# Optimization experiments

Hardware: AMD Instinct MI355X
Metric: run time of the kernel (lower is better)

Reference implementation:

```python
import jax, jax.numpy as jnp
from jax import lax
import numpy as np

B, T, D, H, DH, FF, K = 16, 1024, 512, 8, 64, 2048, 3
EPS = 1e-5


def _layer_norm(x, g, b):
    mu = jnp.mean(x, axis=-1, keepdims=True)
    var = jnp.mean((x - mu) ** 2, axis=-1, keepdims=True)
    return (x - mu) / jnp.sqrt(var + EPS) * g + b


def setup_inputs() -> dict:
    key = jax.random.key(0)
    ks = jax.random.split(key, 14)
    f32 = jnp.float32
    dec_inp = jax.random.normal(ks[0], (B, T, D), f32)
    lengths = jax.random.randint(ks[1], (B,), T // 2, T + 1)
    mask = (jnp.arange(T)[None, :] < lengths[:, None])[:, :, None]  # [B,T,1] bool
    qkv_w = jax.random.normal(ks[2], (3 * H * DH, D), f32) * (D ** -0.5)
    qkv_b = jnp.zeros((3 * H * DH,), f32)
    o_w = jax.random.normal(ks[3], (D, H * DH), f32) * ((H * DH) ** -0.5)
    ln1_g = jnp.ones((D,), f32)
    ln1_b = jnp.zeros((D,), f32)
    conv1_w = jax.random.normal(ks[4], (FF, D, K), f32) * ((D * K) ** -0.5)
    conv1_b = jnp.zeros((FF,), f32)
    conv2_w = jax.random.normal(ks[5], (D, FF, K), f32) * ((FF * K) ** -0.5)
    conv2_b = jnp.zeros((D,), f32)
    ln2_g = jnp.ones((D,), f32)
    ln2_b = jnp.zeros((D,), f32)
    return dict(dec_inp=dec_inp, mask=mask, qkv_w=qkv_w, qkv_b=qkv_b, o_w=o_w,
                ln1_g=ln1_g, ln1_b=ln1_b, conv1_w=conv1_w, conv1_b=conv1_b,
                conv2_w=conv2_w, conv2_b=conv2_b, ln2_g=ln2_g, ln2_b=ln2_b)


def reference(dec_inp, mask, qkv_w, qkv_b, o_w, ln1_g, ln1_b,
              conv1_w, conv1_b, conv2_w, conv2_b, ln2_g, ln2_b):
    # ----- MultiHeadAttn (post-norm, dropout = identity in eval) -----
    attn_mask = ~mask[:, :, 0]                      # [B,T], True = pad
    qkv = dec_inp @ qkv_w.T + qkv_b                 # [B,T,3*H*DH]
    q, k, v = jnp.split(qkv, 3, axis=2)

    def to_heads(x):  # [B,T,H*DH] -> [B*H,T,DH] (batch-major, as in torch)
        return x.reshape(B, T, H, DH).transpose(0, 2, 1, 3).reshape(B * H, T, DH)

    q, k, v = to_heads(q), to_heads(k), to_heads(v)
    scores = jnp.einsum('bqd,bkd->bqk', q, k) * (DH ** -0.5)  # [B*H,T,T]
    # faithful to torch: mask tiled head-major (index i % B)
    am = jnp.tile(attn_mask[:, None, :], (H, T, 1))           # [B*H,T,T]
    scores = jnp.where(am, -jnp.inf, scores)
    prob = jax.nn.softmax(scores, axis=2)
    vec = jnp.einsum('bqk,bkd->bqd', prob, v)                 # [B*H,T,DH]
    # faithful to torch: view as [H,B,...] then permute
    vec = vec.reshape(H, B, T, DH).transpose(1, 2, 0, 3).reshape(B, T, H * DH)
    attn_out = vec @ o_w.T                                    # [B,T,D]
    out = _layer_norm(dec_inp + attn_out, ln1_g, ln1_b)
    out = out * mask

    # ----- PositionwiseConvFF (post-norm) -----
    x = out.transpose(0, 2, 1)                                # [B,D,T]
    h = lax.conv_general_dilated(x, conv1_w, (1,), [(K // 2, K // 2)],
                                 dimension_numbers=('NCH', 'OIH', 'NCH'))
    h = jax.nn.relu(h + conv1_b[None, :, None])
    h = lax.conv_general_dilated(h, conv2_w, (1,), [(K // 2, K // 2)],
                                 dimension_numbers=('NCH', 'OIH', 'NCH'))
    core = (h + conv2_b[None, :, None]).transpose(0, 2, 1)    # [B,T,D]
    out = _layer_norm(out + core, ln2_g, ln2_b)
    return out * mask
```

## Files before the change

### kernel.cpp

```cpp
#include <hip/hip_runtime.h>

using h16 = _Float16;
using h16x4 = __attribute__((ext_vector_type(4))) _Float16;
using h16x8 = __attribute__((ext_vector_type(8))) _Float16;
using f32x4 = __attribute__((ext_vector_type(4))) float;

static constexpr int cB = 16, cT = 1024, cD = 512, cH = 8, cDH = 64, cFF = 2048;
static constexpr int cM = cB * cT;
static constexpr int cTP = cT + 2;

__device__ __forceinline__ bool mask_val(const void* mb, int idx) {
  const unsigned char* u8 = (const unsigned char*)mb;
  if (u8[1] == 1) return u8[idx] != 0;
  const float* f = (const float*)mb;
  if (f[1] == 1.0f) return f[idx] != 0.0f;
  return ((const int*)mb)[idx] != 0;
}

__device__ __forceinline__ void gl_lds16(const h16* g, h16* l) {
  __builtin_amdgcn_global_load_lds(
      (const __attribute__((address_space(1))) unsigned int*)g,
      (__attribute__((address_space(3))) unsigned int*)l, 16, 0, 0);
}


__global__ __launch_bounds__(256) void k_cast4(const float* __restrict__ in,
                                               h16* __restrict__ out, int n4) {
  int i = blockIdx.x * 256 + threadIdx.x;
  if (i >= n4) return;
  const float4 f = ((const float4*)in)[i];
  h16x4 o = {(h16)f.x, (h16)f.y, (h16)f.z, (h16)f.w};
  ((h16x4*)out)[i] = o;
}

__global__ __launch_bounds__(256) void k_repack_w1(const float* __restrict__ w,
                                                   h16* __restrict__ out) {
  int i = blockIdx.x * 256 + threadIdx.x;
  if (i >= cFF * cD) return;
  int f = i >> 9, d = i & 511;
#pragma unroll
  for (int k = 0; k < 3; ++k)
    out[f * (3 * cD) + k * cD + d] = (h16)w[(long)i * 3 + k];
}

__global__ __launch_bounds__(256) void k_repack_w2(const float* __restrict__ w,
                                                   h16* __restrict__ out) {
  int i = blockIdx.x * 256 + threadIdx.x;
  if (i >= cD * cFF) return;
  int o = i >> 11, f = i & 2047;
#pragma unroll
  for (int k = 0; k < 3; ++k)
    out[o * (3 * cFF) + k * cFF + f] = (h16)w[(long)i * 3 + k];
}

__global__ __launch_bounds__(256) void k_zero_pads(h16* __restrict__ xp,
                                                   h16* __restrict__ hp) {
  int i = blockIdx.x * 256 + threadIdx.x;
  if (i < cB * 2 * cD) {
    int b = i / (2 * cD); int rr = (i / cD) & 1; int c = i % cD;
    xp[((long)b * cTP + rr * (cTP - 1)) * cD + c] = (h16)0.f;
  }
  if (i < cB * 2 * cFF) {
    int b = i / (2 * cFF); int rr = (i / cFF) & 1; int c = i % cFF;
    hp[((long)b * cTP + rr * (cTP - 1)) * cFF + c] = (h16)0.f;
  }
}

template <int SKIP, bool A_CONV, bool OUT_CONV, bool BIAS, bool RELU,
          bool OUT_H16, bool VSCAT, int SPLITK, bool SWIZ>
__global__ __launch_bounds__(256)
void gemm_bt(const h16* __restrict__ A, const h16* __restrict__ W,
             const float* __restrict__ bias, void* __restrict__ Cv,
             h16* __restrict__ Vg, const void* __restrict__ maskbuf,
             int ldc, int Kd, int lda, long zstride) {
  __shared__ h16 smem[2 * 128 * 64];
  h16* As = smem;
  h16* Bs = smem + 128 * 64;
  const int tid = threadIdx.x;
  const int w = tid >> 6, l = tid & 63;
  int m0, n0;
  if (SWIZ) {
    m0 = (blockIdx.x * 16 + (blockIdx.y >> 2)) * 128;
    n0 = (blockIdx.y & 3) * 128;
  } else {
    m0 = blockIdx.y * 128;
    n0 = blockIdx.x * 128;
  }

  if (SKIP == 1) {
    if (!mask_val(maskbuf, m0)) return;
  } else if (SKIP == 2) {
    int t0 = m0 & 1023, base = ((m0 >> 10) & 1) * 8;
    bool need = false;
#pragma unroll
    for (int i = 0; i < 8; ++i) need |= mask_val(maskbuf, ((base + i) << 10) + t0);
    if (!need) return;
  } else if (SKIP == 3) {
    int t0 = m0 & 1023;
    if (t0 && !mask_val(maskbuf, m0 - 1)) return;
  }

  const int wm = (w >> 1) * 64, wn = (w & 1) * 64;
  const int lr = l >> 3;
  const int lcs = ((l & 7) ^ lr) * 8;
  const int fr = l & 15;
  const int fb = fr & 7;
  const int qd = l >> 4;

  const int kspan = (SPLITK == 2) ? (Kd >> 1) : Kd;
  const int kbeg = (SPLITK == 2) ? blockIdx.z * kspan : 0;
  const int kend = kbeg + kspan;

  f32x4 zero4 = {0.f, 0.f, 0.f, 0.f};
  f32x4 acc[4][4];
#pragma unroll
  for (int mi = 0; mi < 4; ++mi)
#pragma unroll
    for (int ni = 0; ni < 4; ++ni) acc[mi][ni] = zero4;

  for (int k0 = kbeg; k0 < kend; k0 += 64) {
    __syncthreads();
#pragma unroll
    for (int i = 0; i < 4; ++i) {
      int c = w * 4 + i;
      int ar = m0 + c * 8 + lr;
      long aoff = (long)(ar + (A_CONV ? 2 * (ar >> 10) : 0)) * lda + k0 + lcs;
      gl_lds16(A + aoff, &As[c * 512]);
      int br = n0 + c * 8 + lr;
      long boff = (long)br * Kd + k0 + lcs;
      gl_lds16(W + boff, &Bs[c * 512]);
    }
    __syncthreads();
#pragma unroll
    for (int kc = 0; kc < 2; ++kc) {
      h16x8 af[4], bfr[4];
#pragma unroll
      for (int mi = 0; mi < 4; ++mi)
        af[mi] = *(const h16x8*)&As[(wm + mi * 16 + fr) * 64 +
                                    (((kc * 4 + qd) ^ fb) * 8)];
#pragma unroll
      for (int ni = 0; ni < 4; ++ni)
        bfr[ni] = *(const h16x8*)&Bs[(wn + ni * 16 + fr) * 64 +
                                     (((kc * 4 + qd) ^ fb) * 8)];
#pragma unroll
      for (int mi = 0; mi < 4; ++mi)
#pragma unroll
        for (int ni = 0; ni < 4; ++ni)
          acc[mi][ni] = __builtin_amdgcn_mfma_f32_16x16x32_f16(
              af[mi], bfr[ni], acc[mi][ni], 0, 0, 0);
    }
  }
  const bool do_bias = BIAS && (SPLITK == 1 || blockIdx.z == 0);
  if (VSCAT && n0 >= 1024) {
#pragma unroll
    for (int mi = 0; mi < 4; ++mi) {
      int t0 = (m0 + wm + mi * 16 + (l >> 4) * 4) & 1023;
      int jj = ((m0 >> 10) << 3);
#pragma unroll
      for (int ni = 0; ni < 4; ++ni) {
        int gc = n0 + wn + ni * 16 + fr;
        int dh = gc & 63;
        int j2 = jj + ((gc - 1024) >> 6);
        float bb = do_bias ? bias[gc] : 0.f;
        h16x4 v4 = {(h16)(acc[mi][ni][0] + bb), (h16)(acc[mi][ni][1] + bb),
                    (h16)(acc[mi][ni][2] + bb), (h16)(acc[mi][ni][3] + bb)};
        *(h16x4*)&Vg[((long)j2 * 64 + dh) * 1024 + t0] = v4;
      }
    }
  } else if (OUT_H16) {
    __syncthreads();
#pragma unroll
    for (int mi = 0; mi < 4; ++mi) {
#pragma unroll
      for (int ni = 0; ni < 4; ++ni) {
#pragma unroll
        for (int rr = 0; rr < 4; ++rr) {
          int rrow = wm + mi * 16 + (l >> 4) * 4 + rr;
          int ccol = wn + ni * 16 + fr;
          float v = acc[mi][ni][rr];
          if (do_bias) v += bias[n0 + ccol];
          if (RELU) v = v > 0.f ? v : 0.f;
          smem[rrow * 128 + ccol] = (h16)v;
        }
      }
    }
    __syncthreads();
    h16* outp = (h16*)Cv + (SPLITK == 2 ? (long)blockIdx.z * zstride : 0);
    const int r2 = tid >> 4, c2 = (tid & 15) * 8;
#pragma unroll
    for (int i = 0; i < 8; ++i) {
      int row = r2 + i * 16;
      int gr = m0 + row;
      long orow = (long)gr + (OUT_CONV ? (2 * (gr >> 10) + 1) : 0);
      *(h16x8*)&outp[orow * ldc + n0 + c2] = *(h16x8*)&smem[row * 128 + c2];
    }
  } else {
#pragma unroll
    for (int mi = 0; mi < 4; ++mi) {
#pragma unroll
      for (int ni = 0; ni < 4; ++ni) {
#pragma unroll
        for (int rr = 0; rr < 4; ++rr) {
          int gr = m0 + wm + mi * 16 + (l >> 4) * 4 + rr;
          int gc = n0 + wn + ni * 16 + fr;
          float v = acc[mi][ni][rr];
          if (do_bias) v += bias[gc];
          if (RELU) v = v > 0.f ? v : 0.f;
          long orow = (long)gr + (OUT_CONV ? (2 * (gr >> 10) + 1) : 0);
          ((float*)Cv)[orow * ldc + gc] = v;
        }
      }
    }
  }
}

template <int SKIP, bool A_CONV, bool OUT_CONV, bool BIAS, bool RELU,
          int SPLITK, int NBLK_LOG2>
__global__ __launch_bounds__(1024, 4)
void gemm16(const h16* __restrict__ A, const h16* __restrict__ W,
            const float* __restrict__ bias, h16* __restrict__ C,
            const void* __restrict__ maskbuf, int ldc, int Kd, int lda,
            long zstride) {
  extern __shared__ h16 sm[];
  const int tid = threadIdx.x;
  const int wid = tid >> 6, l = tid & 63;
  const int m0 = (blockIdx.x * 8 + (blockIdx.y >> NBLK_LOG2)) * 256;
  const int n0 = (blockIdx.y & ((1 << NBLK_LOG2) - 1)) * 256;

  if (SKIP == 1) {
    if (!mask_val(maskbuf, m0)) return;
  } else if (SKIP == 3) {
    int t0 = m0 & 1023;
    if (t0 && !mask_val(maskbuf, m0 - 1)) return;
  }

  const int wm = wid >> 2, wn = wid & 3;
  const int fr = l & 15, qd = l >> 4;

  const int kspan = (SPLITK == 2) ? (Kd >> 1) : Kd;
  const int kbeg = (SPLITK == 2) ? blockIdx.z * kspan : 0;
  const int nt = kspan >> 5;

  f32x4 zero4 = {0.f, 0.f, 0.f, 0.f};
  f32x4 acc[4][4];
#pragma unroll
  for (int m = 0; m < 4; ++m)
#pragma unroll
    for (int n = 0; n < 4; ++n) acc[m][n] = zero4;

  const int srow = tid >> 2;
  const int sch = ((tid & 3) - ((tid >> 3) & 3)) & 3;
  const int ar0 = m0 + srow;
  const long aoff0 =
      (long)(ar0 + (A_CONV ? 2 * (ar0 >> 10) : 0)) * lda + kbeg + sch * 8;
  const long boff0 = (long)(n0 + srow) * Kd + kbeg + sch * 8;
  auto stage = [&](int ti) {
    h16* buf = sm + (ti & 3) * 16384;
    gl_lds16(A + aoff0 + ti * 32, &buf[wid * 512]);
    gl_lds16(W + boff0 + ti * 32, &buf[8192 + wid * 512]);
  };

  const int abase = (wm * 64 + fr) * 32 + (((qd + (fr >> 1)) & 3) * 8);
  const int bbase = (wn * 64 + fr) * 32 + (((qd + (fr >> 1)) & 3) * 8);

  stage(0);
  if (nt > 1) stage(1);
  asm volatile("s_waitcnt vmcnt(0)" ::: "memory");
  __builtin_amdgcn_s_barrier();

  for (int s = 0; s < nt; s += 2) {
    if (s + 2 < nt) stage(s + 2);
    if (s + 3 < nt) stage(s + 3);
#pragma unroll
    for (int u = 0; u < 2; ++u) {
      const int t = s + u;
      const h16* Ab = sm + (t & 3) * 16384;
      const h16* Bb = Ab + 8192;
      h16x8 a[4], b[4];
#pragma unroll
      for (int m = 0; m < 4; ++m)
        a[m] = *(const h16x8*)&Ab[abase + m * 512];
#pragma unroll
      for (int n = 0; n < 4; ++n)
        b[n] = *(const h16x8*)&Bb[bbase + n * 512];
      __builtin_amdgcn_s_setprio(1);
#pragma unroll
      for (int m = 0; m < 4; ++m)
#pragma unroll
        for (int n = 0; n < 4; ++n)
          acc[m][n] = __builtin_amdgcn_mfma_f32_16x16x32_f16(a[m], b[n],
                                                             acc[m][n], 0, 0, 0);
      __builtin_amdgcn_s_setprio(0);
    }
    asm volatile("s_waitcnt vmcnt(0)" ::: "memory");
    __builtin_amdgcn_s_barrier();
  }

  const bool do_bias = BIAS && (SPLITK == 1 || blockIdx.z == 0);
  const int qd4 = qd * 4;
#pragma unroll
  for (int m = 0; m < 4; ++m) {
    int row = wm * 64 + m * 16 + qd4;
#pragma unroll
    for (int n = 0; n < 4; ++n) {
      int col = wn * 64 + n * 16 + fr;
      float bb = do_bias ? bias[n0 + col] : 0.f;
#pragma unroll
      for (int rr = 0; rr < 4; ++rr) {
        float v = acc[m][n][rr] + bb;
        if (RELU) v = v > 0.f ? v : 0.f;
        sm[(row + rr) * 256 + col] = (h16)v;
      }
    }
  }
  __syncthreads();
  h16* outp = C + (SPLITK == 2 ? (long)blockIdx.z * zstride : 0);
  const int r2 = tid >> 5, c2 = (tid & 31) * 8;
#pragma unroll
  for (int i = 0; i < 8; ++i) {
    int row = r2 + i * 32;
    int gr = m0 + row;
    long orow = (long)gr + (OUT_CONV ? (2 * (gr >> 10) + 1) : 0);
    *(h16x8*)&outp[orow * (long)ldc + n0 + c2] = *(h16x8*)&sm[row * 256 + c2];
  }
}

__global__ __launch_bounds__(256)
void k_attn(const h16* __restrict__ qk, const h16* __restrict__ Vg,
            const void* __restrict__ maskbuf, h16* __restrict__ attn_out) {
  __shared__ h16 Ks[64 * 64];
  __shared__ h16 Vt[64 * 64];
  __shared__ h16 Ps[4][16 * 68];
  __shared__ float sbias[64];
  const int tid = threadIdx.x, w = tid >> 6, l = tid & 63;
  const int f = blockIdx.x;
  const int bp = f & 15, qt = (f >> 4) & 15, hp = f >> 8;
  const int j = hp * 16 + bp;
  const int bd = j >> 3, hd = j & 7;

  if (!mask_val(maskbuf, bp * cT + qt * 64)) return;

  const int fr = l & 15, fq = (l >> 4) * 8;
  const int fb = fr & 7, qd = l >> 4;
  const int lr = l >> 3, lcs = ((l & 7) ^ lr) * 8;

  h16x8 qf[2];
#pragma unroll
  for (int kc = 0; kc < 2; ++kc) {
    qf[kc] = *(const h16x8*)&qk[
        (long)((bd << 10) + qt * 64 + w * 16 + fr) * 1024 +
        hd * 64 + kc * 32 + fq];
    qf[kc] *= (h16)0.125f;
  }

  f32x4 zero4 = {0.f, 0.f, 0.f, 0.f};
  f32x4 o[4];
  float lrow[4];
#pragma unroll
  for (int nt = 0; nt < 4; ++nt) o[nt] = zero4;
#pragma unroll
  for (int r = 0; r < 4; ++r) lrow[r] = 0.f;

  for (int k0 = 0; k0 < cT; k0 += 64) {
    if (!mask_val(maskbuf, bp * cT + k0)) break;
    __syncthreads();
#pragma unroll
    for (int i = 0; i < 2; ++i) {
      int c = w * 2 + i;
      int row = c * 8 + lr;
      gl_lds16(qk + (long)((bd << 10) + k0 + row) * 1024 + 512 + hd * 64 + lcs,
               &Ks[c * 512]);
      gl_lds16(Vg + ((long)j * 64 + row) * 1024 + k0 + lcs, &Vt[c * 512]);
    }
    if (tid < 64)
      sbias[tid] = mask_val(maskbuf, bp * cT + k0 + tid) ? 0.f : -1e30f;
    __syncthreads();

    f32x4 S[4];
#pragma unroll
    for (int kt = 0; kt < 4; ++kt) {
      float sb = sbias[kt * 16 + fr];
      f32x4 s = {sb, sb, sb, sb};
#pragma unroll
      for (int kc = 0; kc < 2; ++kc) {
        h16x8 kf = *(const h16x8*)&Ks[(kt * 16 + fr) * 64 +
                                      (((kc * 4 + qd) ^ fb) * 8)];
        s = __builtin_amdgcn_mfma_f32_16x16x32_f16(qf[kc], kf, s, 0, 0, 0);
      }
      S[kt] = s;
    }
#pragma unroll
    for (int r = 0; r < 4; ++r) {
      float p0 = __expf(S[0][r] - 4.f), p1 = __expf(S[1][r] - 4.f);
      float p2 = __expf(S[2][r] - 4.f), p3 = __expf(S[3][r] - 4.f);
      lrow[r] += (p0 + p1) + (p2 + p3);
      int ql = (l >> 4) * 4 + r;
      Ps[w][ql * 68 + fr] = (h16)p0;
      Ps[w][ql * 68 + 16 + fr] = (h16)p1;
      Ps[w][ql * 68 + 32 + fr] = (h16)p2;
      Ps[w][ql * 68 + 48 + fr] = (h16)p3;
    }
#pragma unroll
    for (int kp = 0; kp < 2; ++kp) {
      h16x8 pf = *(const h16x8*)&Ps[w][fr * 68 + kp * 32 + fq];
#pragma unroll
      for (int nt = 0; nt < 4; ++nt) {
        h16x8 vf = *(const h16x8*)&Vt[(nt * 16 + fr) * 64 +
                                      (((kp * 4 + qd) ^ fb) * 8)];
        o[nt] = __builtin_amdgcn_mfma_f32_16x16x32_f16(pf, vf, o[nt], 0, 0, 0);
      }
    }
  }
#pragma unroll
  for (int r = 0; r < 4; ++r) {
#pragma unroll
    for (int m = 1; m < 16; m <<= 1) lrow[r] += __shfl_xor(lrow[r], m);
    float inv = 1.f / lrow[r];
    int q = qt * 64 + w * 16 + (l >> 4) * 4 + r;
    long row = (long)bp * cT + q;
#pragma unroll
    for (int nt = 0; nt < 4; ++nt)
      attn_out[row * cD + hp * 64 + nt * 16 + fr] = (h16)(o[nt][r] * inv);
  }
}

template <bool WRITE_XP, bool RH16, bool R2H16>
__global__ __launch_bounds__(256)
void k_ln(const float* __restrict__ X, const void* __restrict__ Rv,
          const void* __restrict__ Rv2,
          const float* __restrict__ g, const float* __restrict__ bta,
          const void* __restrict__ maskbuf,
          float* __restrict__ outf, h16* __restrict__ xp) {
  const int w = threadIdx.x >> 6, l = threadIdx.x & 63;
  const long row = (long)blockIdx.x * 4 + w;
  const float4* x4 = (const float4*)(X + row * cD);
  float4 a0 = x4[l], a1 = x4[l + 64];
  float v[8];
  if (RH16) {
    const h16x4* r4 = (const h16x4*)((const h16*)Rv + row * cD);
    h16x4 b0 = r4[l], b1 = r4[l + 64];
    v[0] = a0.x + (float)b0[0]; v[1] = a0.y + (float)b0[1];
    v[2] = a0.z + (float)b0[2]; v[3] = a0.w + (float)b0[3];
    v[4] = a1.x + (float)b1[0]; v[5] = a1.y + (float)b1[1];
    v[6] = a1.z + (float)b1[2]; v[7] = a1.w + (float)b1[3];
  } else {
    const float4* r4 = (const float4*)((const float*)Rv + row * cD);
    float4 b0 = r4[l], b1 = r4[l + 64];
    v[0] = a0.x + b0.x; v[1] = a0.y + b0.y; v[2] = a0.z + b0.z; v[3] = a0.w + b0.w;
    v[4] = a1.x + b1.x; v[5] = a1.y + b1.y; v[6] = a1.z + b1.z; v[7] = a1.w + b1.w;
  }
  if (R2H16) {
    const h16x4* r4 = (const h16x4*)((const h16*)Rv2 + row * cD);
    h16x4 b0 = r4[l], b1 = r4[l + 64];
    v[0] += (float)b0[0]; v[1] += (float)b0[1];
    v[2] += (float)b0[2]; v[3] += (float)b0[3];
    v[4] += (float)b1[0]; v[5] += (float)b1[1];
    v[6] += (float)b1[2]; v[7] += (float)b1[3];
  }
  float s = 0.f;
#pragma unroll
  for (int i = 0; i < 8; ++i) s += v[i];
#pragma unroll
  for (int m = 1; m < 64; m <<= 1) s += __shfl_xor(s, m);
  const float mu = s * (1.f / 512.f);
  float s2 = 0.f;
#pragma unroll
  for (int i = 0; i < 8; ++i) { float d = v[i] - mu; s2 += d * d; }
#pragma unroll
  for (int m = 1; m < 64; m <<= 1) s2 += __shfl_xor(s2, m);
  const float rstd = rsqrtf(s2 * (1.f / 512.f) + 1e-5f);
  const float mv = mask_val(maskbuf, (int)row) ? 1.f : 0.f;
  const float4* g4 = (const float4*)g;
  const float4* t4 = (const float4*)bta;
  float4 g0 = g4[l], g1 = g4[l + 64], t0 = t4[l], t1 = t4[l + 64];
  float4 y0, y1;
  y0.x = ((v[0] - mu) * rstd * g0.x + t0.x) * mv;
  y0.y = ((v[1] - mu) * rstd * g0.y + t0.y) * mv;
  y0.z = ((v[2] - mu) * rstd * g0.z + t0.z) * mv;
  y0.w = ((v[3] - mu) * rstd * g0.w + t0.w) * mv;
  y1.x = ((v[4] - mu) * rstd * g1.x + t1.x) * mv;
  y1.y = ((v[5] - mu) * rstd * g1.y + t1.y) * mv;
  y1.z = ((v[6] - mu) * rstd * g1.z + t1.z) * mv;
  y1.w = ((v[7] - mu) * rstd * g1.w + t1.w) * mv;
  ((float4*)(outf + row * cD))[l] = y0;
  ((float4*)(outf + row * cD))[l + 64] = y1;
  if (WRITE_XP) {
    const long xrow = row + 2 * (row >> 10) + 1;
    h16x4 h0 = {(h16)y0.x, (h16)y0.y, (h16)y0.z, (h16)y0.w};
    h16x4 h1 = {(h16)y1.x, (h16)y1.y, (h16)y1.z, (h16)y1.w};
    ((h16x4*)(xp + xrow * cD))[l] = h0;
    ((h16x4*)(xp + xrow * cD))[l + 64] = h1;
  }
}

extern "C" void kernel_launch(void* const* d_in, const int* in_sizes, int n_in,
                              void* d_out, int out_size, void* d_ws, size_t ws_size,
                              hipStream_t stream) {
  const float* dec   = (const float*)d_in[0];
  const void*  maskb = d_in[1];
  const float* qkv_w = (const float*)d_in[2];
  const float* qkv_b = (const float*)d_in[3];
  const float* o_w   = (const float*)d_in[4];
  const float* ln1g  = (const float*)d_in[5];
  const float* ln1b  = (const float*)d_in[6];
  const float* c1w   = (const float*)d_in[7];
  const float* c1b   = (const float*)d_in[8];
  const float* c2w   = (const float*)d_in[9];
  const float* c2b   = (const float*)d_in[10];
  const float* ln2g  = (const float*)d_in[11];
  const float* ln2b  = (const float*)d_in[12];

  char* p = (char*)d_ws;
  auto alloc = [&](size_t bytes) {
    char* r = p; p += (bytes + 255) & ~(size_t)255; return r;
  };
  h16*   dec_h  = (h16*)alloc((size_t)cM * cD * 2);
  h16*   qkvw_h = (h16*)alloc((size_t)1536 * cD * 2);
  h16*   ow_h   = (h16*)alloc((size_t)cD * cD * 2);
  h16*   w1p    = (h16*)alloc((size_t)cFF * 3 * cD * 2);
  h16*   w2p    = (h16*)alloc((size_t)cD * 3 * cFF * 2);
  h16*   qk_h   = (h16*)alloc((size_t)cM * 1024 * 2);
  h16*   vg     = (h16*)alloc((size_t)cB * cH * cDH * cT * 2);
  h16*   attn_h = (h16*)alloc((size_t)cM * cD * 2);
  float* tmp    = (float*)alloc((size_t)cM * cD * 4);
  float* out1   = (float*)alloc((size_t)cM * cD * 4);
  h16*   xp     = (h16*)alloc((size_t)cB * cTP * cD * 2);
  h16*   hp     = (h16*)alloc((size_t)cB * cTP * cFF * 2);
  h16*   core0 = attn_h;
  h16*   core1 = qk_h;
  (void)ws_size; (void)n_in; (void)in_sizes; (void)out_size;

  static bool s_attr = false;
  if (!s_attr) {
    hipFuncSetAttribute(
        reinterpret_cast<const void*>(&gemm16<3, true, true, true, true, 1, 3>),
        hipFuncAttributeMaxDynamicSharedMemorySize, 131072);
    hipFuncSetAttribute(
        reinterpret_cast<const void*>(&gemm16<1, true, false, true, false, 2, 1>),
        hipFuncAttributeMaxDynamicSharedMemorySize, 131072);
    s_attr = true;
  }

  k_cast4<<<(cM * cD / 4 + 255) / 256, 256, 0, stream>>>(dec, dec_h, cM * cD / 4);
  k_cast4<<<(1536 * cD / 4 + 255) / 256, 256, 0, stream>>>(qkv_w, qkvw_h, 1536 * cD / 4);
  k_cast4<<<(cD * cD / 4 + 255) / 256, 256, 0, stream>>>(o_w, ow_h, cD * cD / 4);
  k_repack_w1<<<(cFF * cD + 255) / 256, 256, 0, stream>>>(c1w, w1p);
  k_repack_w2<<<(cD * cFF + 255) / 256, 256, 0, stream>>>(c2w, w2p);
  k_zero_pads<<<(cB * 2 * cFF + 255) / 256, 256, 0, stream>>>(xp, hp);

  gemm_bt<2, false, false, true, false, true, true, 1, false>
      <<<dim3(12, cM / 128), 256, 0, stream>>>(dec_h, qkvw_h, qkv_b, qk_h, vg,
                                               maskb, 1024, cD, cD, 0);

  k_attn<<<dim3(2048), 256, 0, stream>>>(qk_h, vg, maskb, attn_h);

  gemm_bt<1, false, false, false, false, false, false, 1, false>
      <<<dim3(cD / 128, cM / 128), 256, 0, stream>>>(attn_h, ow_h, nullptr, tmp,
                                                     nullptr, maskb, cD, cD, cD, 0);

  k_ln<true, false, false><<<cM / 4, 256, 0, stream>>>(dec, tmp, nullptr, ln1g,
                                                       ln1b, maskb, out1, xp);

  gemm16<3, true, true, true, true, 1, 3>
      <<<dim3(8, 64), dim3(1024), 131072, stream>>>(xp, w1p, c1b, hp, maskb,
                                                    cFF, 3 * cD, cD, 0);

  gemm16<1, true, false, true, false, 2, 1>
      <<<dim3(8, 16, 2), dim3(1024), 131072, stream>>>(hp, w2p, c2b, core0,
                                                       maskb, cD, 3 * cFF, cFF,
                                                       (long)(core1 - core0));

  k_ln<false, true, true><<<cM / 4, 256, 0, stream>>>(out1, core0, core1, ln2g,
                                                      ln2b, maskb,
                                                      (float*)d_out, nullptr);
}
```

Baseline: 479.2 us.

## Double-buffer attention K/V tiles and cut fp32 intermediates in the layernorm path

The attention kernel now keeps two LDS buffers for K/V and the mask bias, so the next tile is loaded while the current one is computed, with one barrier per iteration. The loop count comes from a mask scan done up front. The out-projection GEMM now writes fp16 instead of fp32, and LN1 no longer writes an fp32 out1. LN2 reads its residual from the fp16 padded xp buffer, which removes fp32 round-trips at the cost of fp16 rounding on the residual path.

```diff
diff --git a/kernel.cpp b/kernel.cpp
--- a/kernel.cpp
+++ b/kernel.cpp
@@ -328,10 +328,10 @@
 __global__ __launch_bounds__(256)
 void k_attn(const h16* __restrict__ qk, const h16* __restrict__ Vg,
             const void* __restrict__ maskbuf, h16* __restrict__ attn_out) {
-  __shared__ h16 Ks[64 * 64];
-  __shared__ h16 Vt[64 * 64];
+  __shared__ h16 Ks[2][64 * 64];
+  __shared__ h16 Vt[2][64 * 64];
   __shared__ h16 Ps[4][16 * 68];
-  __shared__ float sbias[64];
+  __shared__ float sbias[2][64];
   const int tid = threadIdx.x, w = tid >> 6, l = tid & 63;
   const int f = blockIdx.x;
   const int bp = f & 15, qt = (f >> 4) & 15, hp = f >> 8;
@@ -344,6 +344,10 @@
   const int fb = fr & 7, qd = l >> 4;
   const int lr = l >> 3, lcs = ((l & 7) ^ lr) * 8;
 
+  int nkv = 16;
+  for (int t = 8; t < 16; ++t)
+    if (!mask_val(maskbuf, bp * cT + t * 64)) { nkv = t; break; }
+
   h16x8 qf[2];
 #pragma unroll
   for (int kc = 0; kc < 2; ++kc) {
@@ -353,38 +357,45 @@
     qf[kc] *= (h16)0.125f;
   }
 
-  f32x4 zero4 = {0.f, 0.f, 0.f, 0.f};
-  f32x4 o[4];
-  float lrow[4];
-#pragma unroll
-  for (int nt = 0; nt < 4; ++nt) o[nt] = zero4;
-#pragma unroll
-  for (int r = 0; r < 4; ++r) lrow[r] = 0.f;
-
-  for (int k0 = 0; k0 < cT; k0 += 64) {
-    if (!mask_val(maskbuf, bp * cT + k0)) break;
-    __syncthreads();
+  auto stageKV = [&](int t) {
+    const int buf = t & 1;
+    const int k0 = t * 64;
 #pragma unroll
     for (int i = 0; i < 2; ++i) {
       int c = w * 2 + i;
       int row = c * 8 + lr;
       gl_lds16(qk + (long)((bd << 10) + k0 + row) * 1024 + 512 + hd * 64 + lcs,
-               &Ks[c * 512]);
-      gl_lds16(Vg + ((long)j * 64 + row) * 1024 + k0 + lcs, &Vt[c * 512]);
+               &Ks[buf][c * 512]);
+      gl_lds16(Vg + ((long)j * 64 + row) * 1024 + k0 + lcs, &Vt[buf][c * 512]);
     }
     if (tid < 64)
-      sbias[tid] = mask_val(maskbuf, bp * cT + k0 + tid) ? 0.f : -1e30f;
-    __syncthreads();
+      sbias[buf][tid] = mask_val(maskbuf, bp * cT + k0 + tid) ? 0.f : -1e30f;
+  };
+
+  f32x4 zero4 = {0.f, 0.f, 0.f, 0.f};
+  f32x4 o[4];
+  float lrow[4];
+#pragma unroll
+  for (int nt = 0; nt < 4; ++nt) o[nt] = zero4;
+#pragma unroll
+  for (int r = 0; r < 4; ++r) lrow[r] = 0.f;
+
+  stageKV(0);
+  __syncthreads();
+
+  for (int t = 0; t < nkv; ++t) {
+    const int cur = t & 1;
+    if (t + 1 < nkv) stageKV(t + 1);
 
     f32x4 S[4];
 #pragma unroll
     for (int kt = 0; kt < 4; ++kt) {
-      float sb = sbias[kt * 16 + fr];
+      float sb = sbias[cur][kt * 16 + fr];
       f32x4 s = {sb, sb, sb, sb};
 #pragma unroll
       for (int kc = 0; kc < 2; ++kc) {
-        h16x8 kf = *(const h16x8*)&Ks[(kt * 16 + fr) * 64 +
-                                      (((kc * 4 + qd) ^ fb) * 8)];
+        h16x8 kf = *(const h16x8*)&Ks[cur][(kt * 16 + fr) * 64 +
+                                          (((kc * 4 + qd) ^ fb) * 8)];
         s = __builtin_amdgcn_mfma_f32_16x16x32_f16(qf[kc], kf, s, 0, 0, 0);
       }
       S[kt] = s;
@@ -405,11 +416,12 @@
       h16x8 pf = *(const h16x8*)&Ps[w][fr * 68 + kp * 32 + fq];
 #pragma unroll
       for (int nt = 0; nt < 4; ++nt) {
-        h16x8 vf = *(const h16x8*)&Vt[(nt * 16 + fr) * 64 +
-                                      (((kp * 4 + qd) ^ fb) * 8)];
+        h16x8 vf = *(const h16x8*)&Vt[cur][(nt * 16 + fr) * 64 +
+                                           (((kp * 4 + qd) ^ fb) * 8)];
         o[nt] = __builtin_amdgcn_mfma_f32_16x16x32_f16(pf, vf, o[nt], 0, 0, 0);
       }
     }
+    __syncthreads();
   }
 #pragma unroll
   for (int r = 0; r < 4; ++r) {
@@ -424,30 +436,42 @@
   }
 }
 
-template <bool WRITE_XP, bool RH16, bool R2H16>
+template <bool WRITE_XP, bool RH16, bool R2H16, bool XH16, bool WRITE_OUTF>
 __global__ __launch_bounds__(256)
-void k_ln(const float* __restrict__ X, const void* __restrict__ Rv,
+void k_ln(const void* __restrict__ Xv, const void* __restrict__ Rv,
           const void* __restrict__ Rv2,
           const float* __restrict__ g, const float* __restrict__ bta,
           const void* __restrict__ maskbuf,
           float* __restrict__ outf, h16* __restrict__ xp) {
   const int w = threadIdx.x >> 6, l = threadIdx.x & 63;
   const long row = (long)blockIdx.x * 4 + w;
-  const float4* x4 = (const float4*)(X + row * cD);
-  float4 a0 = x4[l], a1 = x4[l + 64];
   float v[8];
+  if (XH16) {
+    const long xr = row + 2 * (row >> 10) + 1;
+    const h16x4* x4 = (const h16x4*)((const h16*)Xv + xr * cD);
+    h16x4 a0 = x4[l], a1 = x4[l + 64];
+    v[0] = (float)a0[0]; v[1] = (float)a0[1];
+    v[2] = (float)a0[2]; v[3] = (float)a0[3];
+    v[4] = (float)a1[0]; v[5] = (float)a1[1];
+    v[6] = (float)a1[2]; v[7] = (float)a1[3];
+  } else {
+    const float4* x4 = (const float4*)((const float*)Xv + row * cD);
+    float4 a0 = x4[l], a1 = x4[l + 64];
+    v[0] = a0.x; v[1] = a0.y; v[2] = a0.z; v[3] = a0.w;
+    v[4] = a1.x; v[5] = a1.y; v[6] = a1.z; v[7] = a1.w;
+  }
   if (RH16) {
     const h16x4* r4 = (const h16x4*)((const h16*)Rv + row * cD);
     h16x4 b0 = r4[l], b1 = r4[l + 64];
-    v[0] = a0.x + (float)b0[0]; v[1] = a0.y + (float)b0[1];
-    v[2] = a0.z + (float)b0[2]; v[3] = a0.w + (float)b0[3];
-    v[4] = a1.x + (float)b1[0]; v[5] = a1.y + (float)b1[1];
-    v[6] = a1.z + (float)b1[2]; v[7] = a1.w + (float)b1[3];
+    v[0] += (float)b0[0]; v[1] += (float)b0[1];
+    v[2] += (float)b0[2]; v[3] += (float)b0[3];
+    v[4] += (float)b1[0]; v[5] += (float)b1[1];
+    v[6] += (float)b1[2]; v[7] += (float)b1[3];
   } else {
     const float4* r4 = (const float4*)((const float*)Rv + row * cD);
     float4 b0 = r4[l], b1 = r4[l + 64];
-    v[0] = a0.x + b0.x; v[1] = a0.y + b0.y; v[2] = a0.z + b0.z; v[3] = a0.w + b0.w;
-    v[4] = a1.x + b1.x; v[5] = a1.y + b1.y; v[6] = a1.z + b1.z; v[7] = a1.w + b1.w;
+    v[0] += b0.x; v[1] += b0.y; v[2] += b0.z; v[3] += b0.w;
+    v[4] += b1.x; v[5] += b1.y; v[6] += b1.z; v[7] += b1.w;
   }
   if (R2H16) {
     const h16x4* r4 = (const h16x4*)((const h16*)Rv2 + row * cD);
@@ -482,8 +506,10 @@
   y1.y = ((v[5] - mu) * rstd * g1.y + t1.y) * mv;
   y1.z = ((v[6] - mu) * rstd * g1.z + t1.z) * mv;
   y1.w = ((v[7] - mu) * rstd * g1.w + t1.w) * mv;
-  ((float4*)(outf + row * cD))[l] = y0;
-  ((float4*)(outf + row * cD))[l + 64] = y1;
+  if (WRITE_OUTF) {
+    ((float4*)(outf + row * cD))[l] = y0;
+    ((float4*)(outf + row * cD))[l + 64] = y1;
+  }
   if (WRITE_XP) {
     const long xrow = row + 2 * (row >> 10) + 1;
     h16x4 h0 = {(h16)y0.x, (h16)y0.y, (h16)y0.z, (h16)y0.w};
@@ -528,7 +554,8 @@
   h16*   hp     = (h16*)alloc((size_t)cB * cTP * cFF * 2);
   h16*   core0 = attn_h;
   h16*   core1 = qk_h;
-  (void)ws_size; (void)n_in; (void)in_sizes; (void)out_size;
+  h16*   tmp_h = (h16*)tmp;
+  (void)ws_size; (void)n_in; (void)in_sizes; (void)out_size; (void)out1;
 
   static bool s_attr = false;
   if (!s_attr) {
@@ -554,12 +581,12 @@
 
   k_attn<<<dim3(2048), 256, 0, stream>>>(qk_h, vg, maskb, attn_h);
 
-  gemm_bt<1, false, false, false, false, false, false, 1, false>
-      <<<dim3(cD / 128, cM / 128), 256, 0, stream>>>(attn_h, ow_h, nullptr, tmp,
+  gemm_bt<1, false, false, false, false, true, false, 1, false>
+      <<<dim3(cD / 128, cM / 128), 256, 0, stream>>>(attn_h, ow_h, nullptr, tmp_h,
                                                      nullptr, maskb, cD, cD, cD, 0);
 
-  k_ln<true, false, false><<<cM / 4, 256, 0, stream>>>(dec, tmp, nullptr, ln1g,
-                                                       ln1b, maskb, out1, xp);
+  k_ln<true, true, false, false, false><<<cM / 4, 256, 0, stream>>>(
+      dec, tmp_h, nullptr, ln1g, ln1b, maskb, nullptr, xp);
 
   gemm16<3, true, true, true, true, 1, 3>
       <<<dim3(8, 64), dim3(1024), 131072, stream>>>(xp, w1p, c1b, hp, maskb,
@@ -570,7 +597,6 @@
                                                        maskb, cD, 3 * cFF, cFF,
                                                        (long)(core1 - core0));
 
-  k_ln<false, true, true><<<cM / 4, 256, 0, stream>>>(out1, core0, core1, ln2g,
-                                                      ln2b, maskb,
-                                                      (float*)d_out, nullptr);
-}
+  k_ln<false, true, true, true, true><<<cM / 4, 256, 0, stream>>>(
+      xp, core0, core1, ln2g, ln2b, maskb, (float*)d_out, nullptr);
+}
```

New measurement: 482.8 us. About the same (+0.8%).
